# Optimization experiments

Hardware: AMD Instinct MI355X
Metric: run time of the kernel (lower is better)

The kernel has to match this reference:

```python
import jax, jax.numpy as jnp
import numpy as np

SCALE = 1.0

def setup_inputs() -> dict:
    key = jax.random.key(0)
    k1, k2 = jax.random.split(key)
    template = jax.random.normal(k1, (4, 8192, 3), dtype=jnp.float32)
    source = jax.random.normal(k2, (4, 8192, 3), dtype=jnp.float32)
    return {"template": template, "source": source}

def _sq_dist(a, b):
    # a: (B, N, 3), b: (B, M, 3) -> (B, N, M) squared euclidean distances
    a2 = jnp.sum(a * a, axis=-1)  # (B, N)
    b2 = jnp.sum(b * b, axis=-1)  # (B, M)
    ab = jnp.einsum('bnd,bmd->bnm', a, b)  # (B, N, M)
    return a2[:, :, None] - 2.0 * ab + b2[:, None, :]

def reference(template, source):
    p0 = template / SCALE
    p1 = source / SCALE
    d = _sq_dist(p0, p1)  # (B, N, M)
    cost_p0_p1 = jnp.mean(jnp.min(d, axis=2), axis=1)  # (B,)
    cost_p1_p0 = jnp.mean(jnp.min(d, axis=1), axis=1)  # (B,)
    per_batch = cost_p0_p1 + cost_p1_p0  # (B,)
    # reduction='mean'
    return jnp.mean(per_batch, axis=0)
```

## Files before the change

### kernel.cpp

```cpp
#include <hip/hip_runtime.h>
#include <float.h>

#define NPTS   8192
#define NB     4
#define NBDIR  (NB * 2)
#define BLKF   512
#define QPW    32
#define QPB    (8 * QPW)
#define NQB    (NPTS / QPB)
#define STAGE  1024
#define NSTAGE (NPTS / STAGE)
#define BLK    256

typedef __attribute__((ext_vector_type(8)))  short          short8;
typedef __attribute__((ext_vector_type(8)))  unsigned short ushort8;
typedef __attribute__((ext_vector_type(16))) float          f32x16;

__device__ inline unsigned short f2bf(float x) {
  unsigned u = __builtin_bit_cast(unsigned, x);
  u = u + 0x7FFFu + ((u >> 16) & 1u);
  return (unsigned short)(u >> 16);
}
__device__ inline float bf2f(unsigned short h) {
  unsigned u = ((unsigned)h) << 16;
  return __builtin_bit_cast(float, u);
}

__device__ inline ushort8 pack_arow(float x, float y, float z) {
  unsigned short hx = f2bf(x), hy = f2bf(y), hz = f2bf(z);
  unsigned short lx = f2bf(x - bf2f(hx)), ly = f2bf(y - bf2f(hy)),
                 lz = f2bf(z - bf2f(hz));
  ushort8 a = {hx, hy, hz, lx, ly, lz, (unsigned short)0x3F80, 0};
  return a;
}
__device__ inline void pack_brow(float x, float y, float z,
                                 ushort8* blo, ushort8* bhi) {
  unsigned short hx = f2bf(x), hy = f2bf(y), hz = f2bf(z);
  float fx = bf2f(hx), fy = bf2f(hy), fz = bf2f(hz);
  unsigned short lx = f2bf(x - fx), ly = f2bf(y - fy), lz = f2bf(z - fz);
  float s2 = fmaf(x, x, fmaf(y, y, z * z));
  unsigned short s2h = f2bf(s2);
  unsigned short s2l = f2bf(s2 - bf2f(s2h));
  unsigned short nhx = f2bf(-2.0f * fx), nhy = f2bf(-2.0f * fy),
                 nhz = f2bf(-2.0f * fz);
  unsigned short nlx = f2bf(-2.0f * bf2f(lx)), nly = f2bf(-2.0f * bf2f(ly)),
                 nlz = f2bf(-2.0f * bf2f(lz));
  ushort8 lo = {nhx, nhy, nhz, nhx, nhy, nhz, s2h, 0};
  ushort8 hi = {nlx, nly, nlz, nlx, nly, nlz, s2l, 0};
  *blo = lo; *bhi = hi;
}

__global__ __launch_bounds__(BLKF) void chamfer_fused_kernel(
    const float* __restrict__ tpl, const float* __restrict__ src,
    float* __restrict__ partial) {
  __shared__ ushort8 blds8[2 * STAGE];
  __shared__ float red[16];
  const int bd   = blockIdx.x & 7;
  const int qblk = blockIdx.x >> 3;
  const int t = threadIdx.x, w = t >> 6, l = t & 63;
  const int b = bd >> 1, dir = bd & 1;
  const int qbase = qblk * QPB + w * QPW;

  const float* qraw = (dir ? src : tpl) + (size_t)b * NPTS * 3;
  const float* sraw = (dir ? tpl : src) + (size_t)b * NPTS * 3;

  short8 a0;
  {
    int q0 = qbase + (l & 31);
    a0 = __builtin_bit_cast(short8,
        pack_arow(qraw[3 * q0], qraw[3 * q0 + 1], qraw[3 * q0 + 2]));
  }

  f32x16 m0;
  #pragma unroll
  for (int j = 0; j < 16; ++j) m0[j] = FLT_MAX;
  const f32x16 zero = {0.f, 0.f, 0.f, 0.f, 0.f, 0.f, 0.f, 0.f,
                       0.f, 0.f, 0.f, 0.f, 0.f, 0.f, 0.f, 0.f};

  for (int sg = 0; sg < NSTAGE; ++sg) {
    if (sg) __syncthreads();
    #pragma unroll
    for (int i = 0; i < STAGE / BLKF; ++i) {
      int idx = t + BLKF * i;
      int p = sg * STAGE + idx;
      ushort8 blo, bhi;
      pack_brow(sraw[3 * p], sraw[3 * p + 1], sraw[3 * p + 2], &blo, &bhi);
      blds8[idx]         = blo;
      blds8[STAGE + idx] = bhi;
    }
    __syncthreads();

    const int rb = (l >> 5) * STAGE + (l & 31);
    #pragma unroll 4
    for (int st = 0; st < STAGE / 32; ++st) {
      short8 bf = __builtin_bit_cast(short8, blds8[rb + st * 32]);
      f32x16 d0 = __builtin_amdgcn_mfma_f32_32x32x16_bf16(a0, bf, zero, 0, 0, 0);
      #pragma unroll
      for (int j = 0; j < 16; ++j) m0[j] = fminf(m0[j], d0[j]);
    }
  }

  #pragma unroll
  for (int off = 1; off <= 16; off <<= 1) {
    #pragma unroll
    for (int j = 0; j < 16; ++j)
      m0[j] = fminf(m0[j], __shfl_xor(m0[j], off, 64));
  }

  float lsum = 0.0f;
  if ((l & 31) == 0) {
    const int radd = (l >> 5) * 4;
    #pragma unroll
    for (int r = 0; r < 16; ++r) {
      int row = (r & 3) + 8 * (r >> 2) + radd;
      int q = qbase + row;
      float x = qraw[3 * q], y = qraw[3 * q + 1], z = qraw[3 * q + 2];
      lsum += m0[r] + fmaf(x, x, fmaf(y, y, z * z));
    }
    red[w * 2 + (l >> 5)] = lsum;
  }
  __syncthreads();
  if (t == 0) {
    float s = 0.0f;
    #pragma unroll
    for (int i = 0; i < 16; ++i) s += red[i];
    partial[blockIdx.x] = s;
  }
}

__global__ __launch_bounds__(BLK) void final256_kernel(
    const float* __restrict__ partial, float* __restrict__ out) {
  __shared__ float wsum[BLK / 64];
  int t = threadIdx.x;
  float v = partial[t];
  #pragma unroll
  for (int off = 32; off > 0; off >>= 1) v += __shfl_down(v, off, 64);
  if ((t & 63) == 0) wsum[t >> 6] = v;
  __syncthreads();
  if (t == 0)
    out[0] = (wsum[0] + wsum[1] + wsum[2] + wsum[3]) * (1.0f / 32768.0f);
}

#define TILE   2048
#define NTILES (NPTS / TILE)
#define QBLKS  (NPTS / BLK)

__global__ __launch_bounds__(BLK) void chamfer_min_kernel(
    const float* __restrict__ tpl, const float* __restrict__ src,
    float* __restrict__ partial) {
  __shared__ float4 s4[TILE];
  __shared__ float wsum[BLK / 64];
  const int b = blockIdx.z, dir = blockIdx.y;
  const float* qb = (dir == 0 ? tpl : src) + (size_t)b * NPTS * 3;
  const float* rb = (dir == 0 ? src : tpl) + (size_t)b * NPTS * 3;
  const int t = threadIdx.x;
  const int q = blockIdx.x * BLK + t;
  const float qx = qb[3 * q + 0], qy = qb[3 * q + 1], qz = qb[3 * q + 2];
  const float q2 = fmaf(qx, qx, fmaf(qy, qy, qz * qz));
  float b0 = FLT_MAX, b1 = FLT_MAX;
  for (int tile = 0; tile < NTILES; ++tile) {
    const float* rt = rb + 3 * TILE * tile;
    #pragma unroll
    for (int k = 0; k < TILE / BLK; ++k) {
      int p = t + BLK * k;
      float x = rt[3 * p + 0], y = rt[3 * p + 1], z = rt[3 * p + 2];
      s4[p] = make_float4(-2.0f * x, -2.0f * y, -2.0f * z,
                          fmaf(x, x, fmaf(y, y, z * z)));
    }
    __syncthreads();
    #pragma unroll 2
    for (int m = 0; m < TILE; m += 2) {
      float4 p0 = s4[m + 0], p1 = s4[m + 1];
      float d0 = fmaf(qx, p0.x, fmaf(qy, p0.y, fmaf(qz, p0.z, p0.w)));
      float d1 = fmaf(qx, p1.x, fmaf(qy, p1.y, fmaf(qz, p1.z, p1.w)));
      b0 = fminf(b0, fminf(d0, d1));
      b1 = fminf(b1, d0);
    }
    __syncthreads();
  }
  float best = fminf(b0, b1) + q2;
  float v = best;
  #pragma unroll
  for (int off = 32; off > 0; off >>= 1) v += __shfl_down(v, off, 64);
  if ((t & 63) == 0) wsum[t >> 6] = v;
  __syncthreads();
  if (t == 0)
    partial[((b * 2 + dir) * QBLKS) + blockIdx.x] =
        wsum[0] + wsum[1] + wsum[2] + wsum[3];
}

extern "C" void kernel_launch(void* const* d_in, const int* in_sizes, int n_in,
                              void* d_out, int out_size, void* d_ws, size_t ws_size,
                              hipStream_t stream) {
  const float* tpl = (const float*)d_in[0];
  const float* src = (const float*)d_in[1];
  float* out = (float*)d_out;
  float* partial = (float*)d_ws;

  if (ws_size >= 256 * sizeof(float)) {
    chamfer_fused_kernel<<<NBDIR * NQB, BLKF, 0, stream>>>(tpl, src, partial);
    final256_kernel<<<1, BLK, 0, stream>>>(partial, out);
  } else {
    dim3 grid(QBLKS, 2, NB);
    chamfer_min_kernel<<<grid, BLK, 0, stream>>>(tpl, src, partial);
    final256_kernel<<<1, BLK, 0, stream>>>(partial, out);
  }
}
```

Before: 30.22 us.

## Split reference range across two wave groups and double block count

Each block now covers half as many queries, with two groups of four waves each scanning half of every staged reference chunk. Their partial minima are merged through shared memory. This doubles the grid to 512 blocks to improve CU occupancy and latency hiding. The cost is that each reference point is packed into LDS twice as often overall, plus an extra reduction step. The final kernel now sums 512 partials.

```diff
diff --git a/kernel.cpp b/kernel.cpp
--- a/kernel.cpp
+++ b/kernel.cpp
@@ -6,10 +6,11 @@
 #define NBDIR  (NB * 2)
 #define BLKF   512
 #define QPW    32
-#define QPB    (8 * QPW)
+#define QPB    (4 * QPW)
 #define NQB    (NPTS / QPB)
 #define STAGE  1024
 #define NSTAGE (NPTS / STAGE)
+#define HALF   512
 #define BLK    256
 
 typedef __attribute__((ext_vector_type(8)))  short          short8;
@@ -54,12 +55,13 @@
     const float* __restrict__ tpl, const float* __restrict__ src,
     float* __restrict__ partial) {
   __shared__ ushort8 blds8[2 * STAGE];
-  __shared__ float red[16];
+  __shared__ float red[8];
   const int bd   = blockIdx.x & 7;
   const int qblk = blockIdx.x >> 3;
   const int t = threadIdx.x, w = t >> 6, l = t & 63;
+  const int tile = w & 3, rep = w >> 2;
   const int b = bd >> 1, dir = bd & 1;
-  const int qbase = qblk * QPB + w * QPW;
+  const int qbase = qblk * QPB + tile * QPW;
 
   const float* qraw = (dir ? src : tpl) + (size_t)b * NPTS * 3;
   const float* sraw = (dir ? tpl : src) + (size_t)b * NPTS * 3;
@@ -90,9 +92,9 @@
     }
     __syncthreads();
 
-    const int rb = (l >> 5) * STAGE + (l & 31);
+    const int rb = (l >> 5) * STAGE + (l & 31) + rep * HALF;
     #pragma unroll 4
-    for (int st = 0; st < STAGE / 32; ++st) {
+    for (int st = 0; st < HALF / 32; ++st) {
       short8 bf = __builtin_bit_cast(short8, blds8[rb + st * 32]);
       f32x16 d0 = __builtin_amdgcn_mfma_f32_32x32x16_bf16(a0, bf, zero, 0, 0, 0);
       #pragma unroll
@@ -100,39 +102,53 @@
     }
   }
 
-  #pragma unroll
-  for (int off = 1; off <= 16; off <<= 1) {
+  __syncthreads();
+  float* scratch = (float*)blds8;
+  if (rep == 1) {
     #pragma unroll
     for (int j = 0; j < 16; ++j)
-      m0[j] = fminf(m0[j], __shfl_xor(m0[j], off, 64));
-  }
-
-  float lsum = 0.0f;
-  if ((l & 31) == 0) {
-    const int radd = (l >> 5) * 4;
-    #pragma unroll
-    for (int r = 0; r < 16; ++r) {
-      int row = (r & 3) + 8 * (r >> 2) + radd;
-      int q = qbase + row;
-      float x = qraw[3 * q], y = qraw[3 * q + 1], z = qraw[3 * q + 2];
-      lsum += m0[r] + fmaf(x, x, fmaf(y, y, z * z));
-    }
-    red[w * 2 + (l >> 5)] = lsum;
+      scratch[(tile * 64 + l) * 16 + j] = m0[j];
+  }
+  __syncthreads();
+  if (rep == 0) {
+    #pragma unroll
+    for (int j = 0; j < 16; ++j)
+      m0[j] = fminf(m0[j], scratch[(tile * 64 + l) * 16 + j]);
+
+    #pragma unroll
+    for (int off = 1; off <= 16; off <<= 1) {
+      #pragma unroll
+      for (int j = 0; j < 16; ++j)
+        m0[j] = fminf(m0[j], __shfl_xor(m0[j], off, 64));
+    }
+
+    if ((l & 31) == 0) {
+      const int radd = (l >> 5) * 4;
+      float lsum = 0.0f;
+      #pragma unroll
+      for (int r = 0; r < 16; ++r) {
+        int row = (r & 3) + 8 * (r >> 2) + radd;
+        int q = qbase + row;
+        float x = qraw[3 * q], y = qraw[3 * q + 1], z = qraw[3 * q + 2];
+        lsum += m0[r] + fmaf(x, x, fmaf(y, y, z * z));
+      }
+      red[tile * 2 + (l >> 5)] = lsum;
+    }
   }
   __syncthreads();
   if (t == 0) {
     float s = 0.0f;
     #pragma unroll
-    for (int i = 0; i < 16; ++i) s += red[i];
+    for (int i = 0; i < 8; ++i) s += red[i];
     partial[blockIdx.x] = s;
   }
 }
 
-__global__ __launch_bounds__(BLK) void final256_kernel(
+__global__ __launch_bounds__(BLK) void final512_kernel(
     const float* __restrict__ partial, float* __restrict__ out) {
   __shared__ float wsum[BLK / 64];
   int t = threadIdx.x;
-  float v = partial[t];
+  float v = partial[t] + partial[t + 256];
   #pragma unroll
   for (int off = 32; off > 0; off >>= 1) v += __shfl_down(v, off, 64);
   if ((t & 63) == 0) wsum[t >> 6] = v;
@@ -189,6 +205,19 @@
         wsum[0] + wsum[1] + wsum[2] + wsum[3];
 }
 
+__global__ __launch_bounds__(BLK) void final256_kernel(
+    const float* __restrict__ partial, float* __restrict__ out) {
+  __shared__ float wsum[BLK / 64];
+  int t = threadIdx.x;
+  float v = partial[t];
+  #pragma unroll
+  for (int off = 32; off > 0; off >>= 1) v += __shfl_down(v, off, 64);
+  if ((t & 63) == 0) wsum[t >> 6] = v;
+  __syncthreads();
+  if (t == 0)
+    out[0] = (wsum[0] + wsum[1] + wsum[2] + wsum[3]) * (1.0f / 32768.0f);
+}
+
 extern "C" void kernel_launch(void* const* d_in, const int* in_sizes, int n_in,
                               void* d_out, int out_size, void* d_ws, size_t ws_size,
                               hipStream_t stream) {
@@ -197,9 +226,9 @@
   float* out = (float*)d_out;
   float* partial = (float*)d_ws;
 
-  if (ws_size >= 256 * sizeof(float)) {
+  if (ws_size >= 512 * sizeof(float)) {
     chamfer_fused_kernel<<<NBDIR * NQB, BLKF, 0, stream>>>(tpl, src, partial);
-    final256_kernel<<<1, BLK, 0, stream>>>(partial, out);
+    final512_kernel<<<1, BLK, 0, stream>>>(partial, out);
   } else {
     dim3 grid(QBLKS, 2, NB);
     chamfer_min_kernel<<<grid, BLK, 0, stream>>>(tpl, src, partial);
```

New measurement: 32.38 us. 1.07x slower.
